# Kernel tuning notes

Hardware: AMD Instinct MI355X
Metric: run time of the kernel (lower is better)

The kernel has to match this reference:

```python
import jax, jax.numpy as jnp
import numpy as np

FACTOR = 5  # ProbAttention factor


def setup_inputs() -> dict:
    key = jax.random.key(0)
    kq, kk, kv = jax.random.split(key, 3)
    B, H, D, L = 4, 8, 64, 4096
    return {
        "queries": jax.random.normal(kq, (B, H, D, L), jnp.float32),
        "keys": jax.random.normal(kk, (B, H, D, L), jnp.float32),
        "values": jax.random.normal(kv, (B, H, D, L), jnp.float32),
        "attn_mask": jnp.zeros((1,), jnp.bool_),  # unused when mask_flag=True (recomputed internally)
    }


def reference(queries, keys, values, attn_mask):
    B, H, D, L_Q = queries.shape  # input layout [B, H, D, L]
    q = jnp.transpose(queries, (0, 1, 3, 2))  # [B,H,L,D]
    k = jnp.transpose(keys, (0, 1, 3, 2))
    v = jnp.transpose(values, (0, 1, 3, 2))
    L_K = k.shape[2]  # true key length (used inside _prob_QK)
    # --- faithful bug from original: L_K/L_V read from queries' LAST dim (=D) ---
    L_K_bug = D
    L_V_bug = D
    U_part = FACTOR * int(np.ceil(np.log(L_K_bug)))
    U_part = U_part if U_part < L_K_bug else L_K_bug  # sample_k
    u = FACTOR * int(np.ceil(np.log(L_Q)))
    u = u if u < L_Q else L_Q  # n_top
    # scaling (bugged denominators for k, v)
    q = q / (np.sqrt(D) * np.sqrt(L_Q))
    k = k / (np.sqrt(D) * np.sqrt(L_K_bug))
    v = v / (np.sqrt(D) * np.sqrt(L_V_bug))

    # ---- _prob_QK: sampled QK, top-u query selection ----
    skey = jax.random.key(42)  # fixed key: deterministic stand-in for torch.randint
    index_sample = jax.random.randint(skey, (L_Q, U_part), 0, L_K)  # [L_Q, U_part]
    K_sample = k[:, :, index_sample, :]  # [B,H,L_Q,U_part,D]
    Q_K_sample = jnp.einsum('bhld,bhlsd->bhls', q, K_sample)  # [B,H,L_Q,U_part]
    M = Q_K_sample.max(-1) - Q_K_sample.sum(-1) / L_K  # sparsity measure, real L_K here
    _, M_top = jax.lax.top_k(M, u)  # [B,H,u] (order irrelevant: distinct scatter targets)
    Q_reduce = jnp.take_along_axis(q, M_top[..., None], axis=2)  # [B,H,u,D]
    scores = jnp.einsum('bhud,bhkd->bhuk', Q_reduce, k)  # [B,H,u,L_K]

    scale = 1.0 / (np.sqrt(D) * np.sqrt(L_Q))  # self.scale is None
    scores = scores * scale

    # ---- initial context (mask_flag=True -> causal cumsum) ----
    context = jnp.cumsum(v, axis=2)  # [B,H,L_Q,D]

    # ---- ProbMask + update ----
    causal = jnp.triu(jnp.ones((L_Q, L_K), jnp.bool_), 1)  # [L_Q, L_K]
    indicator = causal[M_top]  # [B,H,u,L_K]
    scores = jnp.where(indicator, -jnp.inf, scores)
    attn = jax.nn.softmax(scores, axis=-1)
    upd = jnp.einsum('bhuk,bhkd->bhud', attn, v)  # [B,H,u,D]
    bi = jnp.arange(B)[:, None, None]
    hi = jnp.arange(H)[None, :, None]
    context = context.at[bi, hi, M_top].set(upd)

    out = jnp.transpose(context, (0, 1, 3, 2)).reshape(queries.shape)
    return out
```

## Files before the change

kernel.cpp:

```cpp
#include <hip/hip_runtime.h>
#include <cstdint>

constexpr int B_ = 4, H_ = 8, D_ = 64, L_ = 4096;
constexpr int BH = B_ * H_;
constexpr int U_PART = 25;
constexpr int TOPU = 45;
constexpr int CHUNK = 128;
constexpr int NCH = L_ / CHUNK;
constexpr int PSTRIDE = 68;

#define JAX_THREEFRY_PARTITIONABLE 1

__host__ __device__ inline void tf2x32(uint32_t k0, uint32_t k1,
                                       uint32_t x0, uint32_t x1,
                                       uint32_t& y0, uint32_t& y1) {
  const uint32_t ks2 = k0 ^ k1 ^ 0x1BD11BDAu;
  uint32_t v0 = x0 + k0, v1 = x1 + k1;
#define RND(r) { v0 += v1; v1 = (v1 << (r)) | (v1 >> (32 - (r))); v1 ^= v0; }
  RND(13) RND(15) RND(26) RND(6)
  v0 += k1; v1 += ks2 + 1u;
  RND(17) RND(29) RND(16) RND(24)
  v0 += ks2; v1 += k0 + 2u;
  RND(13) RND(15) RND(26) RND(6)
  v0 += k0; v1 += k1 + 3u;
  RND(17) RND(29) RND(16) RND(24)
  v0 += k1; v1 += ks2 + 4u;
  RND(13) RND(15) RND(26) RND(6)
  v0 += ks2; v1 += k0 + 5u;
#undef RND
  y0 = v0; y1 = v1;
}

__global__ __launch_bounds__(256) void transpose_cumsum(
    const float* __restrict__ k, const float* __restrict__ v,
    float* __restrict__ kt, float* __restrict__ out,
    int* __restrict__ idx, uint32_t k2a, uint32_t k2b) {
  const int bh = blockIdx.y;
  const int t = threadIdx.x;
  if (blockIdx.z == 1) {
#if JAX_THREEFRY_PARTITIONABLE
    const int bid = bh * 64 + blockIdx.x;
    if (t < 50) {
      uint32_t y0, y1;
      const uint32_t i = (uint32_t)(bid * 50 + t);
      tf2x32(k2a, k2b, 0u, i, y0, y1);
      idx[bid * 50 + t] = (int)((y0 ^ y1) & 4095u);
    }
#else
    const int bid = bh * 64 + blockIdx.x;
    const int half = (L_ * U_PART) / 2;
    if (t < 25) {
      uint32_t y0, y1;
      const int j = bid * 25 + t;
      tf2x32(k2a, k2b, (uint32_t)j, (uint32_t)(j + half), y0, y1);
      idx[j] = (int)(y0 & 4095u);
      idx[j + half] = (int)(y1 & 4095u);
    }
#endif
    const int row = bh * D_ + blockIdx.x;
    const float* src = v + (size_t)row * L_;
    float* dst = out + (size_t)row * L_;
    float vals[16];
    const float4* s4 = (const float4*)(src + t * 16);
#pragma unroll
    for (int i = 0; i < 4; i++) {
      float4 x = s4[i];
      vals[4 * i + 0] = x.x; vals[4 * i + 1] = x.y;
      vals[4 * i + 2] = x.z; vals[4 * i + 3] = x.w;
    }
    float run = 0.0f;
#pragma unroll
    for (int i = 0; i < 16; i++) { run += vals[i] * (1.0f / 64.0f); vals[i] = run; }
    float x = run;
#pragma unroll
    for (int off = 1; off < 64; off <<= 1) {
      float y = __shfl_up(x, off, 64);
      if ((t & 63) >= off) x += y;
    }
    __shared__ float wtot[4];
    if ((t & 63) == 63) wtot[t >> 6] = x;
    __syncthreads();
    float woff = 0.0f;
    for (int w = 0; w < (t >> 6); w++) woff += wtot[w];
    const float excl = x - run + woff;
#pragma unroll
    for (int i = 0; i < 16; i++) vals[i] += excl;
    float4* d4 = (float4*)(dst + t * 16);
#pragma unroll
    for (int i = 0; i < 4; i++)
      d4[i] = make_float4(vals[4 * i], vals[4 * i + 1], vals[4 * i + 2], vals[4 * i + 3]);
    return;
  }
  const int l0 = blockIdx.x * 64;
  __shared__ float tile[64][65];
  const float* s = k + (size_t)bh * D_ * L_ + l0;
  float* d = kt + (size_t)bh * L_ * D_;
  const int rhi = t >> 4, rlo = t & 15;
#pragma unroll
  for (int i = 0; i < 4; i++) {
    const int dd = i * 16 + rhi;
    float4 x = *(const float4*)&s[(size_t)dd * L_ + 4 * rlo];
    tile[dd][4 * rlo + 0] = x.x * (1.0f / 64.0f);
    tile[dd][4 * rlo + 1] = x.y * (1.0f / 64.0f);
    tile[dd][4 * rlo + 2] = x.z * (1.0f / 64.0f);
    tile[dd][4 * rlo + 3] = x.w * (1.0f / 64.0f);
  }
  __syncthreads();
#pragma unroll
  for (int i = 0; i < 4; i++) {
    const int ll = i * 16 + rhi;
    float4 o;
    o.x = tile[4 * rlo + 0][ll];
    o.y = tile[4 * rlo + 1][ll];
    o.z = tile[4 * rlo + 2][ll];
    o.w = tile[4 * rlo + 3][ll];
    *(float4*)&d[(size_t)(l0 + ll) * D_ + 4 * rlo] = o;
  }
}

__device__ __forceinline__ float dpp_bcast_add16(float x) {
  int xi;
  xi = __builtin_amdgcn_mov_dpp(__float_as_int(x), 0x140, 0xF, 0xF, true);
  x += __int_as_float(xi);
  xi = __builtin_amdgcn_mov_dpp(__float_as_int(x), 0x141, 0xF, 0xF, true);
  x += __int_as_float(xi);
  xi = __builtin_amdgcn_mov_dpp(__float_as_int(x), 0x4E, 0xF, 0xF, true);
  x += __int_as_float(xi);
  xi = __builtin_amdgcn_mov_dpp(__float_as_int(x), 0xB1, 0xF, 0xF, true);
  x += __int_as_float(xi);
  return x;
}

__global__ __launch_bounds__(1024) void m_kernel(const float* __restrict__ qraw,
                                                 const float* __restrict__ kt,
                                                 const int* __restrict__ idx,
                                                 float* __restrict__ M) {
  const int t = threadIdx.x;
  const int xcd = blockIdx.x & 7;
  const int slot = blockIdx.x >> 3;
  const int bh = xcd * 4 + (slot >> 6);
  const int l0 = (slot & 63) * 64;
  const float* ktb = kt + (size_t)bh * L_ * D_;
  __shared__ float qs[64][65];
  {
    const float* s = qraw + (size_t)bh * D_ * L_ + l0;
    const int w = t >> 6, lane = t & 63;
#pragma unroll
    for (int j = 0; j < 4; j++) {
      const int d = j * 16 + w;
      qs[lane][d] = s[(size_t)d * L_ + lane] * (1.0f / 512.0f);
    }
  }
  __syncthreads();
  const int grp = t >> 4, gl = t & 15;
  const int l = l0 + grp;
  const float4 ql = *(const float4*)&qs[grp][4 * gl];
  const int* ip = idx + (size_t)l * U_PART;
  float mx = -INFINITY, sm = 0.0f;
#pragma unroll 5
  for (int s2 = 0; s2 < U_PART; s2++) {
    const int ki = ip[s2];
    float4 kk = *(const float4*)(ktb + (size_t)ki * D_ + gl * 4);
    float p = ql.x * kk.x + ql.y * kk.y + ql.z * kk.z + ql.w * kk.w;
    p = dpp_bcast_add16(p);
    mx = fmaxf(mx, p);
    sm += p;
  }
  if (gl == 0) M[bh * L_ + l] = mx - sm * (1.0f / 4096.0f);
}

__global__ __launch_bounds__(256) void topk_kernel(const float* __restrict__ M,
                                                   const float* __restrict__ qraw,
                                                   int* __restrict__ ssel_g,
                                                   float* __restrict__ qsel) {
  const int bh = blockIdx.x, t = threadIdx.x;
  const int w = t >> 6, lane = t & 63;
  const float* Mb = M + (size_t)bh * L_;
  const int base = w * 1024 + lane;
  uint32_t v[16];
#pragma unroll
  for (int j = 0; j < 16; j++) {
    uint32_t b = __float_as_uint(Mb[base + j * 64]);
    v[j] = b ^ ((b & 0x80000000u) ? 0xFFFFFFFFu : 0x80000000u);
  }
  __shared__ unsigned long long red[4];
  __shared__ int picks[TOPU];
  __shared__ int ssorted[TOPU];
  for (int it = 0; it < TOPU; it++) {
    unsigned long long best = 0ull;
#pragma unroll
    for (int j = 0; j < 16; j++) {
      unsigned long long key = ((unsigned long long)v[j] << 32)
                             | (uint32_t)(L_ - 1 - (base + j * 64));
      best = (key > best) ? key : best;
    }
#pragma unroll
    for (int off = 32; off; off >>= 1) {
      unsigned long long o = __shfl_xor(best, off, 64);
      best = (o > best) ? o : best;
    }
    if (lane == 0) red[w] = best;
    __syncthreads();
    unsigned long long g = red[0];
    if (red[1] > g) g = red[1];
    if (red[2] > g) g = red[2];
    if (red[3] > g) g = red[3];
    const int bi = L_ - 1 - (int)(g & 0xFFFFFFFFu);
    if (t == 0) picks[it] = bi;
    if ((bi >> 10) == w && (bi & 63) == lane) {
      const int slot = (bi >> 6) & 15;
#pragma unroll
      for (int j = 0; j < 16; j++) if (slot == j) v[j] = 0u;
    }
    __syncthreads();
  }
  if (t < TOPU) {
    int my = picks[t];
    int rank = 0;
    for (int j = 0; j < TOPU; j++) rank += (picks[j] > my);
    ssorted[rank] = my;
  }
  __syncthreads();
  if (t < TOPU) ssel_g[bh * TOPU + t] = ssorted[t];
  const float* qb = qraw + (size_t)bh * D_ * L_;
  for (int e = t; e < TOPU * 64; e += 256) {
    const int r = e >> 6, d = e & 63;
    qsel[((size_t)bh * TOPU + r) * 64 + e % 64] =
        qb[(size_t)d * L_ + ssorted[r]] * (1.0f / 512.0f);
  }
}

__global__ __launch_bounds__(256) void update_partial(const float* __restrict__ qsel,
                                                      const float* __restrict__ kraw,
                                                      const float* __restrict__ vraw,
                                                      const int* __restrict__ ssel_g,
                                                      float* __restrict__ part) {
  const int xcd = blockIdx.x & 7;
  const int slot = blockIdx.x >> 3;
  const int bh = xcd * 4 + (slot >> 4);
  const int ch0 = slot & 15;
  const int t = threadIdx.x;
  const int w = t >> 6, lane = t & 63;
  const int kl = lane & 15, rg = lane >> 4;

  __shared__ float kv[CHUNK * 64];
  __shared__ float qs[48 * 68];
  __shared__ float eS[48 * 132];
  __shared__ int ssel[48];

  if (t < 48) ssel[t] = (t < TOPU) ? ssel_g[bh * TOPU + t] : -1;
  __syncthreads();

#pragma unroll
  for (int j = 0; j < 3; j++) {
    int it = t + 256 * j;
    int rr = it >> 4, dc = it & 15;
    float4 qv = make_float4(0.f, 0.f, 0.f, 0.f);
    if (rr < TOPU) qv = *(const float4*)&qsel[((size_t)bh * TOPU + rr) * 64 + 4 * dc];
    *(float4*)&qs[rr * 68 + 4 * dc] = qv;
  }

  for (int pass = 0; pass < 2; pass++) {
    const int ch = pass ? (31 - ch0) : ch0;
    const int k0 = ch * CHUNK;
    int lo = 0, hi = TOPU;
    while (lo < hi) { int mid = (lo + hi) >> 1; if (ssel[mid] >= k0) lo = mid + 1; else hi = mid; }
    const int nact = lo;
    if (nact == 0) continue;

    __syncthreads();
    const float* kb = kraw + (size_t)bh * D_ * L_ + k0;
#pragma unroll
    for (int j = 0; j < 8; j++) {
      int e4 = 4 * (t + 256 * j);
      int d = e4 >> 7, key = e4 & 127;
      *(float4*)&kv[e4] = *(const float4*)&kb[(size_t)d * L_ + key];
    }
    __syncthreads();

    const int wr0 = 12 * w;
    if (wr0 < nact) {
      float s[3][8];
#pragma unroll
      for (int j = 0; j < 3; j++)
#pragma unroll
        for (int x = 0; x < 8; x++) s[j][x] = 0.f;
#pragma unroll 8
      for (int d = 0; d < 64; d++) {
        float4 ka = *(const float4*)&kv[d * 128 + 4 * kl];
        float4 kb2 = *(const float4*)&kv[d * 128 + 64 + 4 * kl];
#pragma unroll
        for (int j = 0; j < 3; j++) {
          float qd = qs[(wr0 + 3 * rg + j) * 68 + d];
          s[j][0] += qd * ka.x;  s[j][1] += qd * ka.y;
          s[j][2] += qd * ka.z;  s[j][3] += qd * ka.w;
          s[j][4] += qd * kb2.x; s[j][5] += qd * kb2.y;
          s[j][6] += qd * kb2.z; s[j][7] += qd * kb2.w;
        }
      }
#pragma unroll
      for (int j = 0; j < 3; j++) {
        const int R = wr0 + 3 * rg + j;
        const int sel = ssel[R];
        float mx = -INFINITY;
#pragma unroll
        for (int x = 0; x < 8; x++) {
          int kg = k0 + 4 * kl + (x < 4 ? x : 60 + x);
          s[j][x] *= (1.0f / 32768.0f);
          if (kg > sel) s[j][x] = -INFINITY;
          mx = fmaxf(mx, s[j][x]);
        }
        mx = fmaxf(mx, __shfl_xor(mx, 1, 64));
        mx = fmaxf(mx, __shfl_xor(mx, 2, 64));
        mx = fmaxf(mx, __shfl_xor(mx, 4, 64));
        mx = fmaxf(mx, __shfl_xor(mx, 8, 64));
        float e[8], sm = 0.f;
#pragma unroll
        for (int x = 0; x < 8; x++) { e[x] = expf(s[j][x] - mx); sm += e[x]; }
        sm += __shfl_xor(sm, 1, 64);
        sm += __shfl_xor(sm, 2, 64);
        sm += __shfl_xor(sm, 4, 64);
        sm += __shfl_xor(sm, 8, 64);
        *(float4*)&eS[R * 132 + 4 * kl] = make_float4(e[0], e[1], e[2], e[3]);
        *(float4*)&eS[R * 132 + 64 + 4 * kl] = make_float4(e[4], e[5], e[6], e[7]);
        if (kl == 0 && R < nact) {
          float* p = part + ((size_t)(bh * TOPU + R) * NCH + ch) * PSTRIDE;
          p[64] = mx; p[65] = sm;
        }
      }
    }
    __syncthreads();
    const float* vb = vraw + (size_t)bh * D_ * L_ + k0;
#pragma unroll
    for (int j = 0; j < 8; j++) {
      int e4 = 4 * (t + 256 * j);
      int d = e4 >> 7, kq = (e4 & 127) >> 2;
      float4 vv = *(const float4*)&vb[(size_t)d * L_ + 4 * kq];
      *(float4*)&kv[d * 128 + ((kq ^ (d & 31)) << 2)] = vv;
    }
    __syncthreads();
    if (wr0 < nact) {
      float acc[3][4];
#pragma unroll
      for (int j = 0; j < 3; j++)
#pragma unroll
        for (int x = 0; x < 4; x++) acc[j][x] = 0.f;
      const int dbase = 4 * kl;
#pragma unroll 4
      for (int kb = 0; kb < 32; kb++) {
        float4 ev[3];
#pragma unroll
        for (int j = 0; j < 3; j++)
          ev[j] = *(const float4*)&eS[(wr0 + 3 * rg + j) * 132 + 4 * kb];
#pragma unroll
        for (int x = 0; x < 4; x++) {
          const int dx = dbase + x;
          float4 vv = *(const float4*)&kv[dx * 128 + ((kb ^ (dx & 31)) << 2)];
#pragma unroll
          for (int j = 0; j < 3; j++) {
            acc[j][x] += ev[j].x * vv.x + ev[j].y * vv.y
                       + ev[j].z * vv.z + ev[j].w * vv.w;
          }
        }
      }
#pragma unroll
      for (int j = 0; j < 3; j++) {
        const int R = wr0 + 3 * rg + j;
        if (R < nact) {
          float* p = part + ((size_t)(bh * TOPU + R) * NCH + ch) * PSTRIDE;
          float4 o = make_float4(acc[j][0] * (1.0f / 64.0f), acc[j][1] * (1.0f / 64.0f),
                                 acc[j][2] * (1.0f / 64.0f), acc[j][3] * (1.0f / 64.0f));
          *(float4*)&p[4 * kl] = o;
        }
      }
    }
  }
}

__global__ __launch_bounds__(256) void update_combine(const float* __restrict__ part,
                                                      const int* __restrict__ ssel_g,
                                                      float* __restrict__ out) {
  const int row = blockIdx.x * 4 + (threadIdx.x >> 6);
  if (row >= BH * TOPU) return;
  const int bh = row / TOPU;
  const int sel = ssel_g[row];
  const int d = threadIdx.x & 63;
  const int nv = sel / CHUNK + 1;
  const float* p = part + (size_t)row * NCH * PSTRIDE;

  float m = -INFINITY;
  for (int c = 0; c < nv; c++) m = fmaxf(m, p[c * PSTRIDE + 64]);

  float num = 0.0f, den = 0.0f;
  for (int c = 0; c < nv; c++) {
    float mc = p[c * PSTRIDE + 64];
    float wgt = expf(mc - m);
    num += wgt * p[c * PSTRIDE + d];
    den += wgt * p[c * PSTRIDE + 65];
  }
  out[((size_t)bh * D_ + d) * L_ + sel] = num / den;
}

extern "C" void kernel_launch(void* const* d_in, const int* in_sizes, int n_in,
                              void* d_out, int out_size, void* d_ws, size_t ws_size,
                              hipStream_t stream) {
  const float* q = (const float*)d_in[0];
  const float* k = (const float*)d_in[1];
  const float* v = (const float*)d_in[2];
  float* out = (float*)d_out;

  const size_t NT = (size_t)BH * L_ * D_;
  float* kt = (float*)d_ws;
  float* M  = kt + NT;
  int* idx  = (int*)(M + (size_t)BH * L_);
  int* ssel = idx + L_ * U_PART;
  float* qsel = (float*)(ssel + BH * TOPU);
  float* part = qsel + (size_t)BH * TOPU * 64;

  uint32_t k2a, k2b;
#if JAX_THREEFRY_PARTITIONABLE
  tf2x32(0u, 42u, 0u, 1u, k2a, k2b);
#else
  uint32_t a0, a1, b0, b1;
  tf2x32(0u, 42u, 0u, 2u, a0, a1);
  tf2x32(0u, 42u, 1u, 3u, b0, b1);
  k2a = a1; k2b = b1;
#endif

  transpose_cumsum<<<dim3(L_ / 64, BH, 2), 256, 0, stream>>>(k, v, kt, out, idx, k2a, k2b);
  m_kernel<<<BH * 64, 1024, 0, stream>>>(q, kt, idx, M);
  topk_kernel<<<BH, 256, 0, stream>>>(M, q, ssel, qsel);
  update_partial<<<BH * 16, 256, 0, stream>>>(qsel, k, v, ssel, part);
  update_combine<<<(BH * TOPU + 3) / 4, 256, 0, stream>>>(part, ssel, out);
}
```

Measured before the change: 160.9 us.

## Move V cumsum into M kernel blocks to overlap with sampled QK work

The causal cumsum over V moves out of the transpose/RNG prep kernel and into the sparsity-measure kernel. Every fifth block of a 2560-block grid now does cumsum over four rows, and the other blocks keep the M computation with a remapped XCD-aware block-to-(bh, l0) assignment. The cumsum loads and stores also become nontemporal. The aim is to run the memory-bound cumsum alongside the gather-heavy M work and to shrink the prep kernel, at the cost of more complex block indexing and a syncthreads that the whole 1024-thread block must reach in the cumsum branch.

```diff
diff --git a/kernel.cpp b/kernel.cpp
--- a/kernel.cpp
+++ b/kernel.cpp
@@ -10,6 +10,8 @@
 constexpr int PSTRIDE = 68;
 
 #define JAX_THREEFRY_PARTITIONABLE 1
+
+typedef float f4v __attribute__((ext_vector_type(4)));
 
 __host__ __device__ inline void tf2x32(uint32_t k0, uint32_t k1,
                                        uint32_t x0, uint32_t x1,
@@ -31,14 +33,13 @@
   y0 = v0; y1 = v1;
 }
 
-__global__ __launch_bounds__(256) void transpose_cumsum(
-    const float* __restrict__ k, const float* __restrict__ v,
-    float* __restrict__ kt, float* __restrict__ out,
+__global__ __launch_bounds__(256) void prep_kernel(
+    const float* __restrict__ k, float* __restrict__ kt,
     int* __restrict__ idx, uint32_t k2a, uint32_t k2b) {
   const int bh = blockIdx.y;
   const int t = threadIdx.x;
-  if (blockIdx.z == 1) {
 #if JAX_THREEFRY_PARTITIONABLE
+  {
     const int bid = bh * 64 + blockIdx.x;
     if (t < 50) {
       uint32_t y0, y1;
@@ -46,7 +47,9 @@
       tf2x32(k2a, k2b, 0u, i, y0, y1);
       idx[bid * 50 + t] = (int)((y0 ^ y1) & 4095u);
     }
+  }
 #else
+  {
     const int bid = bh * 64 + blockIdx.x;
     const int half = (L_ * U_PART) / 2;
     if (t < 25) {
@@ -56,41 +59,8 @@
       idx[j] = (int)(y0 & 4095u);
       idx[j + half] = (int)(y1 & 4095u);
     }
+  }
 #endif
-    const int row = bh * D_ + blockIdx.x;
-    const float* src = v + (size_t)row * L_;
-    float* dst = out + (size_t)row * L_;
-    float vals[16];
-    const float4* s4 = (const float4*)(src + t * 16);
-#pragma unroll
-    for (int i = 0; i < 4; i++) {
-      float4 x = s4[i];
-      vals[4 * i + 0] = x.x; vals[4 * i + 1] = x.y;
-      vals[4 * i + 2] = x.z; vals[4 * i + 3] = x.w;
-    }
-    float run = 0.0f;
-#pragma unroll
-    for (int i = 0; i < 16; i++) { run += vals[i] * (1.0f / 64.0f); vals[i] = run; }
-    float x = run;
-#pragma unroll
-    for (int off = 1; off < 64; off <<= 1) {
-      float y = __shfl_up(x, off, 64);
-      if ((t & 63) >= off) x += y;
-    }
-    __shared__ float wtot[4];
-    if ((t & 63) == 63) wtot[t >> 6] = x;
-    __syncthreads();
-    float woff = 0.0f;
-    for (int w = 0; w < (t >> 6); w++) woff += wtot[w];
-    const float excl = x - run + woff;
-#pragma unroll
-    for (int i = 0; i < 16; i++) vals[i] += excl;
-    float4* d4 = (float4*)(dst + t * 16);
-#pragma unroll
-    for (int i = 0; i < 4; i++)
-      d4[i] = make_float4(vals[4 * i], vals[4 * i + 1], vals[4 * i + 2], vals[4 * i + 3]);
-    return;
-  }
   const int l0 = blockIdx.x * 64;
   __shared__ float tile[64][65];
   const float* s = k + (size_t)bh * D_ * L_ + l0;
@@ -131,17 +101,61 @@
   return x;
 }
 
-__global__ __launch_bounds__(1024) void m_kernel(const float* __restrict__ qraw,
-                                                 const float* __restrict__ kt,
-                                                 const int* __restrict__ idx,
-                                                 float* __restrict__ M) {
+__global__ __launch_bounds__(1024) void m_cumsum_kernel(
+    const float* __restrict__ qraw, const float* __restrict__ kt,
+    const int* __restrict__ idx, const float* __restrict__ vraw,
+    float* __restrict__ M, float* __restrict__ out) {
+  const int bid = blockIdx.x;
   const int t = threadIdx.x;
-  const int xcd = blockIdx.x & 7;
-  const int slot = blockIdx.x >> 3;
-  const int bh = xcd * 4 + (slot >> 6);
-  const int l0 = (slot & 63) * 64;
+  __shared__ float qs[64][65];
+  __shared__ float wtot[4][4];
+  if (bid % 5 == 4) {
+    const int slot = bid / 5;
+    const int sg = t >> 8;
+    const int t2 = t & 255;
+    const int row = slot * 4 + sg;
+    const float* src = vraw + (size_t)row * L_;
+    float* dst = out + (size_t)row * L_;
+    float vals[16];
+    const f4v* s4 = (const f4v*)(src + t2 * 16);
+#pragma unroll
+    for (int i = 0; i < 4; i++) {
+      f4v x = __builtin_nontemporal_load(&s4[i]);
+      vals[4 * i + 0] = x.x; vals[4 * i + 1] = x.y;
+      vals[4 * i + 2] = x.z; vals[4 * i + 3] = x.w;
+    }
+    float run = 0.0f;
+#pragma unroll
+    for (int i = 0; i < 16; i++) { run += vals[i] * (1.0f / 64.0f); vals[i] = run; }
+    float x = run;
+#pragma unroll
+    for (int off = 1; off < 64; off <<= 1) {
+      float y = __shfl_up(x, off, 64);
+      if ((t2 & 63) >= off) x += y;
+    }
+    if ((t2 & 63) == 63) wtot[sg][t2 >> 6] = x;
+    __syncthreads();
+    float woff = 0.0f;
+    for (int w = 0; w < (t2 >> 6); w++) woff += wtot[sg][w];
+    const float excl = x - run + woff;
+#pragma unroll
+    for (int i = 0; i < 16; i++) vals[i] += excl;
+    f4v* d4 = (f4v*)(dst + t2 * 16);
+#pragma unroll
+    for (int i = 0; i < 4; i++) {
+      f4v o = {vals[4 * i], vals[4 * i + 1], vals[4 * i + 2], vals[4 * i + 3]};
+      __builtin_nontemporal_store(o, &d4[i]);
+    }
+    return;
+  }
+  const int xcd = bid & 7;
+  const int c = bid % 40;
+  const int rbad_tbl[8] = {24, 9, 34, 19, 4, 29, 14, 39};
+  const int rank = (c >> 3) - (rbad_tbl[xcd] < c ? 1 : 0);
+  const int o = (bid / 40) * 4 + rank;
+  const int bh = xcd * 4 + (o >> 6);
+  const int l0 = (o & 63) * 64;
   const float* ktb = kt + (size_t)bh * L_ * D_;
-  __shared__ float qs[64][65];
   {
     const float* s = qraw + (size_t)bh * D_ * L_ + l0;
     const int w = t >> 6, lane = t & 63;
@@ -427,8 +441,8 @@
   k2a = a1; k2b = b1;
 #endif
 
-  transpose_cumsum<<<dim3(L_ / 64, BH, 2), 256, 0, stream>>>(k, v, kt, out, idx, k2a, k2b);
-  m_kernel<<<BH * 64, 1024, 0, stream>>>(q, kt, idx, M);
+  prep_kernel<<<dim3(L_ / 64, BH), 256, 0, stream>>>(k, kt, idx, k2a, k2b);
+  m_cumsum_kernel<<<2560, 1024, 0, stream>>>(q, kt, idx, v, M, out);
   topk_kernel<<<BH, 256, 0, stream>>>(M, q, ssel, qsel);
   update_partial<<<BH * 16, 256, 0, stream>>>(qsel, k, v, ssel, part);
   update_combine<<<(BH * TOPU + 3) / 4, 256, 0, stream>>>(part, ssel, out);
```

New measurement: 173.4 us. 1.08x slower.

## Move value cumsum from prep kernel into top-k kernel as extra blocks

Applied to the files above, without the earlier changes.

The causal cumsum of values no longer runs as half of the first (transpose/index) kernel's grid. It now runs as extra blocks appended to the top-k kernel's launch. The top-k step alone launches only 32 blocks and leaves most of the GPU idle, so the cumsum work can fill those idle compute units instead of lengthening the prep stage. One risk is that the topk blocks get scheduled late or compete with the cumsum blocks for bandwidth. Another is that the merged kernel's shared-memory and register footprint reduces occupancy.

```diff
diff --git a/kernel.cpp b/kernel.cpp
--- a/kernel.cpp
+++ b/kernel.cpp
@@ -31,14 +31,13 @@
   y0 = v0; y1 = v1;
 }
 
-__global__ __launch_bounds__(256) void transpose_cumsum(
-    const float* __restrict__ k, const float* __restrict__ v,
-    float* __restrict__ kt, float* __restrict__ out,
+__global__ __launch_bounds__(256) void prep_kernel(
+    const float* __restrict__ k, float* __restrict__ kt,
     int* __restrict__ idx, uint32_t k2a, uint32_t k2b) {
   const int bh = blockIdx.y;
   const int t = threadIdx.x;
-  if (blockIdx.z == 1) {
 #if JAX_THREEFRY_PARTITIONABLE
+  {
     const int bid = bh * 64 + blockIdx.x;
     if (t < 50) {
       uint32_t y0, y1;
@@ -46,7 +45,9 @@
       tf2x32(k2a, k2b, 0u, i, y0, y1);
       idx[bid * 50 + t] = (int)((y0 ^ y1) & 4095u);
     }
+  }
 #else
+  {
     const int bid = bh * 64 + blockIdx.x;
     const int half = (L_ * U_PART) / 2;
     if (t < 25) {
@@ -56,41 +57,8 @@
       idx[j] = (int)(y0 & 4095u);
       idx[j + half] = (int)(y1 & 4095u);
     }
+  }
 #endif
-    const int row = bh * D_ + blockIdx.x;
-    const float* src = v + (size_t)row * L_;
-    float* dst = out + (size_t)row * L_;
-    float vals[16];
-    const float4* s4 = (const float4*)(src + t * 16);
-#pragma unroll
-    for (int i = 0; i < 4; i++) {
-      float4 x = s4[i];
-      vals[4 * i + 0] = x.x; vals[4 * i + 1] = x.y;
-      vals[4 * i + 2] = x.z; vals[4 * i + 3] = x.w;
-    }
-    float run = 0.0f;
-#pragma unroll
-    for (int i = 0; i < 16; i++) { run += vals[i] * (1.0f / 64.0f); vals[i] = run; }
-    float x = run;
-#pragma unroll
-    for (int off = 1; off < 64; off <<= 1) {
-      float y = __shfl_up(x, off, 64);
-      if ((t & 63) >= off) x += y;
-    }
-    __shared__ float wtot[4];
-    if ((t & 63) == 63) wtot[t >> 6] = x;
-    __syncthreads();
-    float woff = 0.0f;
-    for (int w = 0; w < (t >> 6); w++) woff += wtot[w];
-    const float excl = x - run + woff;
-#pragma unroll
-    for (int i = 0; i < 16; i++) vals[i] += excl;
-    float4* d4 = (float4*)(dst + t * 16);
-#pragma unroll
-    for (int i = 0; i < 4; i++)
-      d4[i] = make_float4(vals[4 * i], vals[4 * i + 1], vals[4 * i + 2], vals[4 * i + 3]);
-    return;
-  }
   const int l0 = blockIdx.x * 64;
   __shared__ float tile[64][65];
   const float* s = k + (size_t)bh * D_ * L_ + l0;
@@ -169,11 +137,49 @@
   if (gl == 0) M[bh * L_ + l] = mx - sm * (1.0f / 4096.0f);
 }
 
-__global__ __launch_bounds__(256) void topk_kernel(const float* __restrict__ M,
-                                                   const float* __restrict__ qraw,
-                                                   int* __restrict__ ssel_g,
-                                                   float* __restrict__ qsel) {
-  const int bh = blockIdx.x, t = threadIdx.x;
+__global__ __launch_bounds__(256) void topk_cumsum_kernel(
+    const float* __restrict__ M, const float* __restrict__ qraw,
+    const float* __restrict__ vraw,
+    int* __restrict__ ssel_g, float* __restrict__ qsel,
+    float* __restrict__ out) {
+  const int bid = blockIdx.x;
+  const int t = threadIdx.x;
+  if (bid >= BH) {
+    const int row = bid - BH;
+    const float* src = vraw + (size_t)row * L_;
+    float* dst = out + (size_t)row * L_;
+    float vals[16];
+    const float4* s4 = (const float4*)(src + t * 16);
+#pragma unroll
+    for (int i = 0; i < 4; i++) {
+      float4 x = s4[i];
+      vals[4 * i + 0] = x.x; vals[4 * i + 1] = x.y;
+      vals[4 * i + 2] = x.z; vals[4 * i + 3] = x.w;
+    }
+    float run = 0.0f;
+#pragma unroll
+    for (int i = 0; i < 16; i++) { run += vals[i] * (1.0f / 64.0f); vals[i] = run; }
+    float x = run;
+#pragma unroll
+    for (int off = 1; off < 64; off <<= 1) {
+      float y = __shfl_up(x, off, 64);
+      if ((t & 63) >= off) x += y;
+    }
+    __shared__ float wtot[4];
+    if ((t & 63) == 63) wtot[t >> 6] = x;
+    __syncthreads();
+    float woff = 0.0f;
+    for (int w = 0; w < (t >> 6); w++) woff += wtot[w];
+    const float excl = x - run + woff;
+#pragma unroll
+    for (int i = 0; i < 16; i++) vals[i] += excl;
+    float4* d4 = (float4*)(dst + t * 16);
+#pragma unroll
+    for (int i = 0; i < 4; i++)
+      d4[i] = make_float4(vals[4 * i], vals[4 * i + 1], vals[4 * i + 2], vals[4 * i + 3]);
+    return;
+  }
+  const int bh = bid;
   const int w = t >> 6, lane = t & 63;
   const float* Mb = M + (size_t)bh * L_;
   const int base = w * 1024 + lane;
@@ -427,9 +433,9 @@
   k2a = a1; k2b = b1;
 #endif
 
-  transpose_cumsum<<<dim3(L_ / 64, BH, 2), 256, 0, stream>>>(k, v, kt, out, idx, k2a, k2b);
+  prep_kernel<<<dim3(L_ / 64, BH), 256, 0, stream>>>(k, kt, idx, k2a, k2b);
   m_kernel<<<BH * 64, 1024, 0, stream>>>(q, kt, idx, M);
-  topk_kernel<<<BH, 256, 0, stream>>>(M, q, ssel, qsel);
+  topk_cumsum_kernel<<<BH + BH * D_, 256, 0, stream>>>(M, q, v, ssel, qsel, out);
   update_partial<<<BH * 16, 256, 0, stream>>>(qsel, k, v, ssel, part);
   update_combine<<<(BH * TOPU + 3) / 4, 256, 0, stream>>>(part, ssel, out);
 }
```

After: 149.3 us, median of 2. 1.08x faster.
